# Kernel tuning notes

Hardware: AMD Instinct MI355X
Metric: run time of the kernel (lower is better)

## Reference

```python
import jax, jax.numpy as jnp
import numpy as np

B, N, D = 4, 4096, 1024
H, S, R = 16, 256, 2           # heads, segment size, dilation rate
DH = D // H
LN_EPS = 1e-5


def _hilbert_perm(n_side):
    # perm[d] = linear index (y*side + x) of the d-th point on the Hilbert curve
    def d2xy(n, d):
        x = y = 0
        t = d
        s = 1
        while s < n:
            rx = 1 & (t // 2)
            ry = 1 & (t ^ rx)
            if ry == 0:
                if rx == 1:
                    x = s - 1 - x
                    y = s - 1 - y
                x, y = y, x
            x += s * rx
            y += s * ry
            t //= 4
            s *= 2
        return x, y
    perm = np.empty(n_side * n_side, dtype=np.int32)
    for d in range(n_side * n_side):
        xx, yy = d2xy(n_side, d)
        perm[d] = yy * n_side + xx
    return perm


def setup_inputs() -> dict:
    key = jax.random.key(0)
    ks = jax.random.split(key, 8)
    sc = 0.02
    return {
        "x": jax.random.normal(ks[0], (B, N, D), jnp.float32),
        "ln1_g": jnp.ones((D,), jnp.float32),
        "ln1_b": jnp.zeros((D,), jnp.float32),
        "w_qkv": jax.random.normal(ks[1], (D, 3 * D), jnp.float32) * sc,
        "b_qkv": jnp.zeros((3 * D,), jnp.float32),
        "w_o": jax.random.normal(ks[2], (D, D), jnp.float32) * sc,
        "b_o": jnp.zeros((D,), jnp.float32),
        "ln2_g": jnp.ones((D,), jnp.float32),
        "ln2_b": jnp.zeros((D,), jnp.float32),
        "w1": jax.random.normal(ks[3], (D, 4 * D), jnp.float32) * sc,
        "b1": jnp.zeros((4 * D,), jnp.float32),
        "w2": jax.random.normal(ks[4], (4 * D, D), jnp.float32) * sc,
        "b2": jnp.zeros((D,), jnp.float32),
        "hilbert_perm": jnp.asarray(_hilbert_perm(int(np.sqrt(N)))),
    }


def _layernorm(x, g, b):
    mu = jnp.mean(x, axis=-1, keepdims=True)
    var = jnp.mean(jnp.square(x - mu), axis=-1, keepdims=True)
    return (x - mu) * jax.lax.rsqrt(var + LN_EPS) * g + b


def _hilbert_dilated_attention(x, w_qkv, b_qkv, w_o, b_o, perm):
    b, n, d = x.shape
    nseg, sr = n // S, S // R
    xp = jnp.take(x, perm, axis=1)                    # Hilbert reorder
    qkv = xp @ w_qkv + b_qkv                          # [b,n,3d]
    q, k, v = jnp.split(qkv, 3, axis=-1)
    def seg(t):
        return t.reshape(b, nseg, S, H, DH)
    q, k, v = seg(q), seg(k), seg(v)
    # per-head dilation offset: head h attends positions (h % R) :: R in each segment
    offs = jnp.arange(H, dtype=jnp.int32) % R                        # [H]
    idx = offs[None, :] + R * jnp.arange(sr, dtype=jnp.int32)[:, None]  # [sr,H]
    idx_g = idx[None, None, :, :, None]                              # [1,1,sr,H,1]
    qd = jnp.take_along_axis(q, idx_g, axis=2)        # [b,nseg,sr,H,dh]
    kd = jnp.take_along_axis(k, idx_g, axis=2)
    vd = jnp.take_along_axis(v, idx_g, axis=2)
    scores = jnp.einsum('bgqhd,bgkhd->bghqk', qd, kd) / jnp.sqrt(jnp.asarray(DH, x.dtype))
    attn = jax.nn.softmax(scores, axis=-1)
    od = jnp.einsum('bghqk,bgkhd->bgqhd', attn, vd)   # [b,nseg,sr,H,dh]
    # scatter back into full segments; uncovered (head,pos) slots stay zero
    out = jnp.zeros((b, nseg, S, H, DH), x.dtype)
    out = out.at[:, :, idx, jnp.arange(H)[None, :], :].set(od)
    out = out.reshape(b, n, d) @ w_o + b_o
    inv = jnp.argsort(perm)
    return jnp.take(out, inv, axis=1)                 # inverse Hilbert reorder


def reference(x, ln1_g, ln1_b, w_qkv, b_qkv, w_o, b_o, ln2_g, ln2_b, w1, b1, w2, b2, hilbert_perm):
    h = _layernorm(x, ln1_g, ln1_b)
    h = _hilbert_dilated_attention(h, w_qkv, b_qkv, w_o, b_o, hilbert_perm)
    x = x + h
    h = _layernorm(x, ln2_g, ln2_b)
    h = jax.nn.gelu(h @ w1 + b1, approximate=False) @ w2 + b2
    return x + h
```

## Files before the change

### kernel.cpp

```cpp
#include <hip/hip_runtime.h>

typedef short bf16x8 __attribute__((ext_vector_type(8)));
typedef float f32x4 __attribute__((ext_vector_type(4)));
typedef unsigned short u16;

#define GLDS16(g, l) __builtin_amdgcn_global_load_lds( \
    (const __attribute__((address_space(1))) void*)(g), \
    (__attribute__((address_space(3))) void*)(l), 16, 0, 0)

__device__ __forceinline__ u16 f2b(float f) {
  unsigned u = __float_as_uint(f);
  u += 0x7fffu + ((u >> 16) & 1u);
  return (u16)(u >> 16);
}

__global__ __launch_bounds__(256)
void transpose_bf16(const float* __restrict__ w, u16* __restrict__ wt, int K, int N) {
  __shared__ float tile[32][33];
  const int n0 = blockIdx.x * 32, k0 = blockIdx.y * 32;
  const int tx = threadIdx.x & 31, ty = threadIdx.x >> 5;
#pragma unroll
  for (int i = 0; i < 4; ++i)
    tile[ty + i * 8][tx] = w[(size_t)(k0 + ty + i * 8) * N + n0 + tx];
  __syncthreads();
#pragma unroll
  for (int i = 0; i < 4; ++i)
    wt[(size_t)(n0 + ty + i * 8) * K + k0 + tx] = f2b(tile[tx][ty + i * 8]);
}

__global__ __launch_bounds__(256)
void ln_rows(const float* __restrict__ src, const float* __restrict__ gam,
             const float* __restrict__ bet, const int* __restrict__ perm,
             u16* __restrict__ dst) {
  const int orow = blockIdx.x;
  const int b = orow >> 12, j = orow & 4095;
  const int srow = perm ? ((b << 12) + perm[j]) : orow;
  const float4 v = ((const float4*)(src + (size_t)srow * 1024))[threadIdx.x];
  float s = v.x + v.y + v.z + v.w;
  float s2 = v.x * v.x + v.y * v.y + v.z * v.z + v.w * v.w;
#pragma unroll
  for (int d = 1; d < 64; d <<= 1) { s += __shfl_xor(s, d); s2 += __shfl_xor(s2, d); }
  __shared__ float rs[4], rs2[4];
  const int wave = threadIdx.x >> 6, lane = threadIdx.x & 63;
  if (lane == 0) { rs[wave] = s; rs2[wave] = s2; }
  __syncthreads();
  s = rs[0] + rs[1] + rs[2] + rs[3];
  s2 = rs2[0] + rs2[1] + rs2[2] + rs2[3];
  const float mu = s * (1.f / 1024.f);
  const float var = s2 * (1.f / 1024.f) - mu * mu;
  const float rstd = rsqrtf(var + 1e-5f);
  const int c = threadIdx.x * 4;
  const float4 gg = *(const float4*)(gam + c);
  const float4 bb = *(const float4*)(bet + c);
  const u16 o0 = f2b((v.x - mu) * rstd * gg.x + bb.x);
  const u16 o1 = f2b((v.y - mu) * rstd * gg.y + bb.y);
  const u16 o2 = f2b((v.z - mu) * rstd * gg.z + bb.z);
  const u16 o3 = f2b((v.w - mu) * rstd * gg.w + bb.w);
  const unsigned lo = (unsigned)o0 | ((unsigned)o1 << 16);
  const unsigned hi = (unsigned)o2 | ((unsigned)o3 << 16);
  *(uint2*)(dst + (size_t)orow * 1024 + c) = make_uint2(lo, hi);
}

template <int EPI>
__global__ __launch_bounds__(512, 2)
void gemm256(const u16* __restrict__ A, const u16* __restrict__ Bt,
             const float* __restrict__ bias, void* __restrict__ Cout,
             const float* __restrict__ resid, const int* __restrict__ perm,
             int M, int Nn, int K) {
  __shared__ u16 sm[65536];
  char* const smc = (char*)sm;
  const int tid = threadIdx.x;
  const int w = tid >> 6, lane = tid & 63;
  const int lr = lane & 15, lg = lane >> 4;
  const int wm = w >> 2, wn = w & 3;

  int wg = blockIdx.x;
  const int nwg = gridDim.x;
  if ((nwg & 7) == 0) { const int per = nwg >> 3; wg = (wg & 7) * per + (wg >> 3); }
  const int gx = M >> 8;
  const int m0 = (wg % gx) << 8, n0 = (wg / gx) << 8;

  const int srow = tid >> 3;
  const int scol = ((tid & 7) ^ (srow & 7)) << 3;
  const size_t aSrc = (size_t)(m0 + srow) * K + scol;
  const size_t bSrc = (size_t)(n0 + srow) * K + scol;
  char* const lWav = smc + w * 1024;

  const int slot0 = (lg ^ (lr & 7)) << 4;
  const int aRow = (wm * 128 + lr) * 128;
  const int bRow = (wn * 64 + lr) * 128 + 32768;

  const int NT = K >> 6;

#define STAGE_(d, mat, h, k0) do { \
    const u16* gp = ((mat) ? Bt : A) + ((mat) ? bSrc : aSrc) + (size_t)(h) * 128 * K + (k0); \
    char* lp = lWav + (d) * 65536 + (mat) * 32768 + (h) * 16384; \
    GLDS16(gp, lp); GLDS16(gp + (size_t)64 * K, lp + 8192); } while (0)

  bf16x8 aLo[8], aHi[8], bLo[4], bHi[4];

#define R_ALO(P) do { _Pragma("unroll") for (int mf = 0; mf < 4; ++mf) \
    _Pragma("unroll") for (int kk = 0; kk < 2; ++kk) \
      aLo[mf * 2 + kk] = *(const bf16x8*)((P) + mf * 2048 + (slot0 ^ (kk << 6))); } while (0)
#define R_AHI(P) do { _Pragma("unroll") for (int mf = 0; mf < 4; ++mf) \
    _Pragma("unroll") for (int kk = 0; kk < 2; ++kk) \
      aHi[mf * 2 + kk] = *(const bf16x8*)((P) + (4 + mf) * 2048 + (slot0 ^ (kk << 6))); } while (0)
#define R_BLO(P) do { _Pragma("unroll") for (int nf = 0; nf < 2; ++nf) \
    _Pragma("unroll") for (int kk = 0; kk < 2; ++kk) \
      bLo[nf * 2 + kk] = *(const bf16x8*)((P) + nf * 2048 + (slot0 ^ (kk << 6))); } while (0)
#define R_BHI(P) do { _Pragma("unroll") for (int nf = 0; nf < 2; ++nf) \
    _Pragma("unroll") for (int kk = 0; kk < 2; ++kk) \
      bHi[nf * 2 + kk] = *(const bf16x8*)((P) + (2 + nf) * 2048 + (slot0 ^ (kk << 6))); } while (0)

#define QUAD_(AARR, BARR, MB, NB) do { _Pragma("unroll") for (int mf = 0; mf < 4; ++mf) \
    _Pragma("unroll") for (int nf = 0; nf < 2; ++nf) \
    _Pragma("unroll") for (int kk = 0; kk < 2; ++kk) \
      acc[(MB) * 4 + mf][(NB) * 2 + nf] = __builtin_amdgcn_mfma_f32_16x16x32_bf16( \
          AARR[mf * 2 + kk], BARR[nf * 2 + kk], acc[(MB) * 4 + mf][(NB) * 2 + nf], 0, 0, 0); } while (0)

#define LGKM0SB_() do { asm volatile("s_waitcnt lgkmcnt(0)" ::: "memory"); \
                        __builtin_amdgcn_sched_barrier(0); } while (0)

  STAGE_(0, 1, 0, 0); STAGE_(0, 1, 1, 0); STAGE_(0, 0, 0, 0); STAGE_(0, 0, 1, 0);
  if (NT > 1) {
    STAGE_(1, 1, 0, 64); STAGE_(1, 1, 1, 64); STAGE_(1, 0, 0, 64);
    asm volatile("s_waitcnt vmcnt(6)" ::: "memory");
  } else {
    asm volatile("s_waitcnt vmcnt(0)" ::: "memory");
  }
  __builtin_amdgcn_s_barrier();

  f32x4 acc[8][4] = {};

  for (int t = 0; t < NT; ++t) {
    const int c = t & 1;
    const char* cA = smc + c * 65536 + aRow;
    const char* cB = smc + c * 65536 + bRow;

    R_ALO(cA); R_BLO(cB);
    if (t + 1 < NT) STAGE_(c ^ 1, 0, 1, (t + 1) << 6);
    asm volatile("s_waitcnt lgkmcnt(8)" ::: "memory");
    __builtin_amdgcn_s_barrier();
    LGKM0SB_();
    __builtin_amdgcn_s_setprio(1);
    QUAD_(aLo, bLo, 0, 0);
    __builtin_amdgcn_s_setprio(0);
    __builtin_amdgcn_s_barrier();

    R_BHI(cB);
    if (t + 2 < NT) STAGE_(c, 1, 0, (t + 2) << 6);
    __builtin_amdgcn_s_barrier();
    LGKM0SB_();
    __builtin_amdgcn_s_setprio(1);
    QUAD_(aLo, bHi, 0, 1);
    __builtin_amdgcn_s_setprio(0);
    __builtin_amdgcn_s_barrier();

    R_AHI(cA);
    if (t + 2 < NT) STAGE_(c, 1, 1, (t + 2) << 6);
    __builtin_amdgcn_s_barrier();
    LGKM0SB_();
    __builtin_amdgcn_s_setprio(1);
    QUAD_(aHi, bLo, 1, 0);
    __builtin_amdgcn_s_setprio(0);
    __builtin_amdgcn_s_barrier();

    if (t + 2 < NT) STAGE_(c, 0, 0, (t + 2) << 6);
    if (t < NT - 2) asm volatile("s_waitcnt vmcnt(6)" ::: "memory");
    else            asm volatile("s_waitcnt vmcnt(0)" ::: "memory");
    __builtin_amdgcn_s_barrier();
    __builtin_amdgcn_sched_barrier(0);
    __builtin_amdgcn_s_setprio(1);
    QUAD_(aHi, bHi, 1, 1);
    __builtin_amdgcn_s_setprio(0);
    __builtin_amdgcn_s_barrier();
  }
#undef STAGE_
#undef R_ALO
#undef R_AHI
#undef R_BLO
#undef R_BHI
#undef QUAD_
#undef LGKM0SB_

#pragma unroll
  for (int mf = 0; mf < 8; ++mf) {
#pragma unroll
    for (int nf = 0; nf < 4; ++nf) {
      const int col = n0 + wn * 64 + nf * 16 + lr;
      const float bia = bias[col];
#pragma unroll
      for (int r = 0; r < 4; ++r) {
        const int row = m0 + wm * 128 + mf * 16 + lg * 4 + r;
        float v = acc[mf][nf][r] + bia;
        if (EPI == 0) {
          ((u16*)Cout)[(size_t)row * Nn + col] = f2b(v);
        } else if (EPI == 1) {
          v = 0.5f * v * (1.f + erff(v * 0.70710678118654752f));
          ((u16*)Cout)[(size_t)row * Nn + col] = f2b(v);
        } else if (EPI == 2) {
          const int b = row >> 12, j = row & 4095;
          const size_t di = ((size_t)((b << 12) + perm[j])) * 1024 + col;
          ((float*)Cout)[di] = resid[di] + v;
        } else {
          const size_t di = (size_t)row * 1024 + col;
          ((float*)Cout)[di] = resid[di] + v;
        }
      }
    }
  }
}

__global__ __launch_bounds__(256, 2)
void attn_kernel(const u16* __restrict__ qkv, u16* __restrict__ outp) {
  const int blk = blockIdx.x;
  const int h = blk & 15, g = (blk >> 4) & 15, b = blk >> 8;
  const int tid = threadIdx.x, wave = tid >> 6, lane = tid & 63;
  const int lr = lane & 15, lg = lane >> 4;
  const int par = h & 1;

  __shared__ u16 lQ[128 * 64];
  __shared__ u16 lK[128 * 64];
  __shared__ u16 lVt[64 * 128];
  __shared__ u16 lP[4][32 * 128];

  const size_t rbase = (size_t)((b << 12) + (g << 8) + par);

#pragma unroll
  for (int i = 0; i < 4; ++i) {
    const int ou = i * 4096 + wave * 1024;
    const int o = ou + lane * 16;
    const int j = o >> 7, cb = o & 127;
    const u16* gq = qkv + (rbase + 2 * j) * 3072 + h * 64 + (cb >> 1);
    GLDS16(gq, (char*)lQ + ou);
    GLDS16(gq + 1024, (char*)lK + ou);
  }
#pragma unroll
  for (int i = 0; i < 4; ++i) {
    const int c = tid + i * 256;
    const int j = c >> 3, dc = c & 7;
    const uint4 vv = *(const uint4*)(qkv + (rbase + 2 * j) * 3072 + 2048 + h * 64 + dc * 8);
    const u16* pv = (const u16*)&vv;
#pragma unroll
    for (int e = 0; e < 8; ++e) lVt[(dc * 8 + e) * 128 + j] = pv[e];
  }
  __syncthreads();

  f32x4 sacc[2][8] = {};
#pragma unroll
  for (int kk = 0; kk < 2; ++kk) {
    bf16x8 aq[2], bk[8];
#pragma unroll
    for (int mf = 0; mf < 2; ++mf)
      aq[mf] = *(const bf16x8*)&lQ[(wave * 32 + mf * 16 + lr) * 64 + kk * 32 + lg * 8];
#pragma unroll
    for (int nf = 0; nf < 8; ++nf)
      bk[nf] = *(const bf16x8*)&lK[(nf * 16 + lr) * 64 + kk * 32 + lg * 8];
#pragma unroll
    for (int mf = 0; mf < 2; ++mf)
#pragma unroll
      for (int nf = 0; nf < 8; ++nf)
        sacc[mf][nf] = __builtin_amdgcn_mfma_f32_16x16x32_bf16(aq[mf], bk[nf], sacc[mf][nf], 0, 0, 0);
  }

#pragma unroll
  for (int mf = 0; mf < 2; ++mf) {
#pragma unroll
    for (int r = 0; r < 4; ++r) {
      float mx = -3e38f;
#pragma unroll
      for (int nf = 0; nf < 8; ++nf) mx = fmaxf(mx, sacc[mf][nf][r]);
#pragma unroll
      for (int d = 1; d < 16; d <<= 1) mx = fmaxf(mx, __shfl_xor(mx, d));
      float pv[8];
      float sum = 0.f;
#pragma unroll
      for (int nf = 0; nf < 8; ++nf) {
        pv[nf] = __expf((sacc[mf][nf][r] - mx) * 0.125f);
        sum += pv[nf];
      }
#pragma unroll
      for (int d = 1; d < 16; d <<= 1) sum += __shfl_xor(sum, d);
      const float inv = 1.f / sum;
      const int rrow = mf * 16 + lg * 4 + r;
#pragma unroll
      for (int nf = 0; nf < 8; ++nf)
        lP[wave][rrow * 128 + nf * 16 + lr] = f2b(pv[nf] * inv);
    }
  }
  __syncthreads();

  f32x4 oacc[2][4] = {};
#pragma unroll
  for (int kk = 0; kk < 4; ++kk) {
    bf16x8 ap[2], bv[4];
#pragma unroll
    for (int mf = 0; mf < 2; ++mf)
      ap[mf] = *(const bf16x8*)&lP[wave][(mf * 16 + lr) * 128 + kk * 32 + lg * 8];
#pragma unroll
    for (int nf = 0; nf < 4; ++nf)
      bv[nf] = *(const bf16x8*)&lVt[(nf * 16 + lr) * 128 + kk * 32 + lg * 8];
#pragma unroll
    for (int mf = 0; mf < 2; ++mf)
#pragma unroll
      for (int nf = 0; nf < 4; ++nf)
        oacc[mf][nf] = __builtin_amdgcn_mfma_f32_16x16x32_bf16(ap[mf], bv[nf], oacc[mf][nf], 0, 0, 0);
  }

  u16* obase = outp + ((size_t)((b << 12) + (g << 8))) * 1024 + h * 64;
#pragma unroll
  for (int mf = 0; mf < 2; ++mf)
#pragma unroll
    for (int nf = 0; nf < 4; ++nf)
#pragma unroll
      for (int r = 0; r < 4; ++r) {
        const int jq = wave * 32 + mf * 16 + lg * 4 + r;
        obase[(size_t)(par + 2 * jq) * 1024 + nf * 16 + lr] = f2b(oacc[mf][nf][r]);
      }
  const int jz = tid >> 1, hh = (tid & 1) * 32;
  u16* zp = obase + (size_t)((1 - par) + 2 * jz) * 1024 + hh;
  const uint4 z = make_uint4(0u, 0u, 0u, 0u);
#pragma unroll
  for (int i = 0; i < 4; ++i) ((uint4*)zp)[i] = z;
}

extern "C" void kernel_launch(void* const* d_in, const int* in_sizes, int n_in,
                              void* d_out, int out_size, void* d_ws, size_t ws_size,
                              hipStream_t stream) {
  const float* x    = (const float*)d_in[0];
  const float* ln1g = (const float*)d_in[1];
  const float* ln1b = (const float*)d_in[2];
  const float* wqkv = (const float*)d_in[3];
  const float* bqkv = (const float*)d_in[4];
  const float* wo   = (const float*)d_in[5];
  const float* bo   = (const float*)d_in[6];
  const float* ln2g = (const float*)d_in[7];
  const float* ln2b = (const float*)d_in[8];
  const float* w1   = (const float*)d_in[9];
  const float* b1   = (const float*)d_in[10];
  const float* w2   = (const float*)d_in[11];
  const float* b2   = (const float*)d_in[12];
  const int*   perm = (const int*)d_in[13];
  float* out = (float*)d_out;
  char* ws = (char*)d_ws;

  u16*  r0    = (u16*)ws;
  u16*  qkv   = (u16*)(ws + (32ull << 20));
  u16*  a1    = (u16*)(ws + (32ull << 20));
  float* x2   = (float*)(ws + (160ull << 20));
  u16*  wqkvT = (u16*)(ws + (224ull << 20));
  u16*  woT   = (u16*)(ws + (230ull << 20));
  u16*  w1T   = (u16*)(ws + (232ull << 20));
  u16*  w2T   = (u16*)(ws + (240ull << 20));

  transpose_bf16<<<dim3(3072 / 32, 1024 / 32), 256, 0, stream>>>(wqkv, wqkvT, 1024, 3072);
  transpose_bf16<<<dim3(1024 / 32, 1024 / 32), 256, 0, stream>>>(wo, woT, 1024, 1024);
  transpose_bf16<<<dim3(4096 / 32, 1024 / 32), 256, 0, stream>>>(w1, w1T, 1024, 4096);
  transpose_bf16<<<dim3(1024 / 32, 4096 / 32), 256, 0, stream>>>(w2, w2T, 4096, 1024);

  ln_rows<<<16384, 256, 0, stream>>>(x, ln1g, ln1b, perm, r0);
  gemm256<0><<<(16384 / 256) * (3072 / 256), 512, 0, stream>>>(r0, wqkvT, bqkv, qkv, nullptr, nullptr,
                                                               16384, 3072, 1024);
  attn_kernel<<<1024, 256, 0, stream>>>(qkv, r0);
  gemm256<2><<<(16384 / 256) * (1024 / 256), 512, 0, stream>>>(r0, woT, bo, x2, x, perm,
                                                               16384, 1024, 1024);
  ln_rows<<<16384, 256, 0, stream>>>(x2, ln2g, ln2b, nullptr, r0);
  gemm256<1><<<(16384 / 256) * (4096 / 256), 512, 0, stream>>>(r0, w1T, b1, a1, nullptr, nullptr,
                                                               16384, 4096, 1024);
  gemm256<3><<<(16384 / 256) * (1024 / 256), 512, 0, stream>>>(a1, w2T, b2, out, x2, nullptr,
                                                               16384, 1024, 4096);
}
```

Before: 605.5 us.

## Stage GEMM tiles through registers instead of direct global-to-LDS loads

```diff
diff --git a/kernel.cpp b/kernel.cpp
--- a/kernel.cpp
+++ b/kernel.cpp
@@ -81,10 +81,10 @@
   const int m0 = (wg % gx) << 8, n0 = (wg / gx) << 8;
 
   const int srow = tid >> 3;
-  const int scol = ((tid & 7) ^ (srow & 7)) << 3;
-  const size_t aSrc = (size_t)(m0 + srow) * K + scol;
-  const size_t bSrc = (size_t)(n0 + srow) * K + scol;
-  char* const lWav = smc + w * 1024;
+  const int lin8 = (tid & 7) << 3;
+  const u16* gA = A + (size_t)(m0 + srow) * K + lin8;
+  const u16* gB = Bt + (size_t)(n0 + srow) * K + lin8;
+  const int wslot = ((tid & 7) ^ (srow & 7)) << 4;
 
   const int slot0 = (lg ^ (lr & 7)) << 4;
   const int aRow = (wm * 128 + lr) * 128;
@@ -92,19 +92,25 @@
 
   const int NT = K >> 6;
 
-#define STAGE_(d, mat, h, k0) do { \
-    const u16* gp = ((mat) ? Bt : A) + ((mat) ? bSrc : aSrc) + (size_t)(h) * 128 * K + (k0); \
-    char* lp = lWav + (d) * 65536 + (mat) * 32768 + (h) * 16384; \
-    GLDS16(gp, lp); GLDS16(gp + (size_t)64 * K, lp + 8192); } while (0)
-
-  bf16x8 aLo[8], aHi[8], bLo[4], bHi[4];
+  uint4 astg[4], bstg[4];
+
+#define LOADA_(k0) do { _Pragma("unroll") for (int i = 0; i < 4; ++i) \
+    astg[i] = *(const uint4*)(gA + (size_t)(64 * i) * K + (k0)); } while (0)
+#define LOADB_(k0) do { _Pragma("unroll") for (int i = 0; i < 4; ++i) \
+    bstg[i] = *(const uint4*)(gB + (size_t)(64 * i) * K + (k0)); } while (0)
+#define WRITEAB_(d) do { char* base_ = smc + (d) * 65536; \
+    _Pragma("unroll") for (int i = 0; i < 4; ++i) { \
+      *(uint4*)(base_ + (srow + 64 * i) * 128 + wslot) = astg[i]; \
+      *(uint4*)(base_ + 32768 + (srow + 64 * i) * 128 + wslot) = bstg[i]; } } while (0)
+
+  bf16x8 a[8], bLo[4], bHi[4];
 
 #define R_ALO(P) do { _Pragma("unroll") for (int mf = 0; mf < 4; ++mf) \
     _Pragma("unroll") for (int kk = 0; kk < 2; ++kk) \
-      aLo[mf * 2 + kk] = *(const bf16x8*)((P) + mf * 2048 + (slot0 ^ (kk << 6))); } while (0)
+      a[mf * 2 + kk] = *(const bf16x8*)((P) + mf * 2048 + (slot0 ^ (kk << 6))); } while (0)
 #define R_AHI(P) do { _Pragma("unroll") for (int mf = 0; mf < 4; ++mf) \
     _Pragma("unroll") for (int kk = 0; kk < 2; ++kk) \
-      aHi[mf * 2 + kk] = *(const bf16x8*)((P) + (4 + mf) * 2048 + (slot0 ^ (kk << 6))); } while (0)
+      a[mf * 2 + kk] = *(const bf16x8*)((P) + (4 + mf) * 2048 + (slot0 ^ (kk << 6))); } while (0)
 #define R_BLO(P) do { _Pragma("unroll") for (int nf = 0; nf < 2; ++nf) \
     _Pragma("unroll") for (int kk = 0; kk < 2; ++kk) \
       bLo[nf * 2 + kk] = *(const bf16x8*)((P) + nf * 2048 + (slot0 ^ (kk << 6))); } while (0)
@@ -112,22 +118,20 @@
     _Pragma("unroll") for (int kk = 0; kk < 2; ++kk) \
       bHi[nf * 2 + kk] = *(const bf16x8*)((P) + (2 + nf) * 2048 + (slot0 ^ (kk << 6))); } while (0)
 
-#define QUAD_(AARR, BARR, MB, NB) do { _Pragma("unroll") for (int mf = 0; mf < 4; ++mf) \
+#define QUAD_(BARR, MB, NB) do { _Pragma("unroll") for (int mf = 0; mf < 4; ++mf) \
     _Pragma("unroll") for (int nf = 0; nf < 2; ++nf) \
     _Pragma("unroll") for (int kk = 0; kk < 2; ++kk) \
       acc[(MB) * 4 + mf][(NB) * 2 + nf] = __builtin_amdgcn_mfma_f32_16x16x32_bf16( \
-          AARR[mf * 2 + kk], BARR[nf * 2 + kk], acc[(MB) * 4 + mf][(NB) * 2 + nf], 0, 0, 0); } while (0)
+          a[mf * 2 + kk], BARR[nf * 2 + kk], acc[(MB) * 4 + mf][(NB) * 2 + nf], 0, 0, 0); } while (0)
 
 #define LGKM0SB_() do { asm volatile("s_waitcnt lgkmcnt(0)" ::: "memory"); \
                         __builtin_amdgcn_sched_barrier(0); } while (0)
 
-  STAGE_(0, 1, 0, 0); STAGE_(0, 1, 1, 0); STAGE_(0, 0, 0, 0); STAGE_(0, 0, 1, 0);
-  if (NT > 1) {
-    STAGE_(1, 1, 0, 64); STAGE_(1, 1, 1, 64); STAGE_(1, 0, 0, 64);
-    asm volatile("s_waitcnt vmcnt(6)" ::: "memory");
-  } else {
-    asm volatile("s_waitcnt vmcnt(0)" ::: "memory");
-  }
+  LOADB_(0); LOADA_(0);
+  asm volatile("s_waitcnt vmcnt(0)" ::: "memory");
+  WRITEAB_(0);
+  if (NT > 1) { LOADB_(64); LOADA_(64); }
+  asm volatile("s_waitcnt lgkmcnt(0)" ::: "memory");
   __builtin_amdgcn_s_barrier();
 
   f32x4 acc[8][4] = {};
@@ -138,44 +142,44 @@
     const char* cB = smc + c * 65536 + bRow;
 
     R_ALO(cA); R_BLO(cB);
-    if (t + 1 < NT) STAGE_(c ^ 1, 0, 1, (t + 1) << 6);
-    asm volatile("s_waitcnt lgkmcnt(8)" ::: "memory");
+    if (t + 1 < NT) {
+      asm volatile("s_waitcnt vmcnt(0)" ::: "memory");
+      WRITEAB_(c ^ 1);
+    }
     __builtin_amdgcn_s_barrier();
     LGKM0SB_();
     __builtin_amdgcn_s_setprio(1);
-    QUAD_(aLo, bLo, 0, 0);
+    QUAD_(bLo, 0, 0);
     __builtin_amdgcn_s_setprio(0);
     __builtin_amdgcn_s_barrier();
 
     R_BHI(cB);
-    if (t + 2 < NT) STAGE_(c, 1, 0, (t + 2) << 6);
+    if (t + 2 < NT) LOADB_((t + 2) << 6);
     __builtin_amdgcn_s_barrier();
     LGKM0SB_();
     __builtin_amdgcn_s_setprio(1);
-    QUAD_(aLo, bHi, 0, 1);
+    QUAD_(bHi, 0, 1);
     __builtin_amdgcn_s_setprio(0);
     __builtin_amdgcn_s_barrier();
 
     R_AHI(cA);
-    if (t + 2 < NT) STAGE_(c, 1, 1, (t + 2) << 6);
+    if (t + 2 < NT) LOADA_((t + 2) << 6);
     __builtin_amdgcn_s_barrier();
     LGKM0SB_();
     __builtin_amdgcn_s_setprio(1);
-    QUAD_(aHi, bLo, 1, 0);
+    QUAD_(bLo, 1, 0);
     __builtin_amdgcn_s_setprio(0);
     __builtin_amdgcn_s_barrier();
 
-    if (t + 2 < NT) STAGE_(c, 0, 0, (t + 2) << 6);
-    if (t < NT - 2) asm volatile("s_waitcnt vmcnt(6)" ::: "memory");
-    else            asm volatile("s_waitcnt vmcnt(0)" ::: "memory");
-    __builtin_amdgcn_s_barrier();
     __builtin_amdgcn_sched_barrier(0);
     __builtin_amdgcn_s_setprio(1);
-    QUAD_(aHi, bHi, 1, 1);
+    QUAD_(bHi, 1, 1);
     __builtin_amdgcn_s_setprio(0);
     __builtin_amdgcn_s_barrier();
   }
-#undef STAGE_
+#undef LOADA_
+#undef LOADB_
+#undef WRITEAB_
 #undef R_ALO
 #undef R_AHI
 #undef R_BLO
```

Result: slower. 1.080 ms (+78.4%).
